# Performance work log

Measured on AMD Instinct MI355X. Metric: run time of the kernel, lower is better.

Reference implementation:

```python
import jax, jax.numpy as jnp
import numpy as np
from jax import lax

B, T, D, H, W = 2, 8, 64, 64, 64
E, HID = 4, 256


def _layernorm(x, g, b, eps=1e-5):
    m = x.mean(-1, keepdims=True)
    v = ((x - m) ** 2).mean(-1, keepdims=True)
    return (x - m) / jnp.sqrt(v + eps) * g + b


def _pscan(A, X, axis):
    # linear recurrence h_t = A_t * h_{t-1} + X_t via associative scan
    def comb(l, r):
        a1, x1 = l
        a2, x2 = r
        return a2 * a1, a2 * x1 + x2
    return lax.associative_scan(comb, (A, X), axis=axis)[1]


def setup_inputs() -> dict:
    key = jax.random.key(0)
    ks = jax.random.split(key, 32)
    r = lambda i, shape, s=1.0: jax.random.normal(ks[i], shape, jnp.float32) * s
    D2 = 2 * D
    return {
        'x_re': r(0, (B, T, D, H, W)), 'x_im': r(1, (B, T, D, H, W)),
        'dt': jax.random.uniform(ks[2], (T,), jnp.float32, 0.5, 1.0),
        'ln_s_g': jnp.ones(D2), 'ln_s_b': jnp.zeros(D2),
        'conv_w': r(3, (3, 3, D2, D2), 0.03), 'conv_b': jnp.zeros(D2),
        'mom_w': r(4, (D2, D2), 0.08), 'mom_b': jnp.zeros(D2),
        'adv_w': jnp.full((1,), 0.1, jnp.float32),
        'enc_re': r(5, (D, D), 0.1), 'enc_im': r(6, (D, D), 0.1),
        'dec_re': r(7, (D, D), 0.1), 'dec_im': r(8, (D, D), 0.1),
        'flux_a_re': r(9, (D,)), 'flux_a_im': r(10, (D,), 0.1),
        'fin_re': r(11, (D, D), 0.1), 'fin_im': r(12, (D, D), 0.1),
        'fproj_re': r(13, (D, D), 0.1), 'fproj_im': r(14, (D, D), 0.1),
        'gate_w': r(15, (D2, D), 0.1), 'gate_b': jnp.zeros(D),
        'lam_re': r(16, (D,)), 'lam_im': r(17, (D,), 0.1),
        'noise_re': r(18, (B, T, H, W, D)), 'noise_im': r(19, (B, T, H, W, D)),
        'e_scale': jnp.full((1,), 0.1, jnp.float32),
        'ln_t_g': jnp.ones(D2), 'ln_t_b': jnp.zeros(D2),
        'router_w': r(20, (D2, E), 0.1), 'router_b': jnp.zeros(E),
        'w1': r(21, (E, D2, HID), 0.08), 'b1': jnp.zeros((E, HID)),
        'w2': r(22, (E, HID, D2), 0.08), 'b2': jnp.zeros((E, D2)),
    }


def _forward(x_re, x_im, dt, ln_s_g, ln_s_b, conv_w, conv_b, mom_w, mom_b, adv_w,
             enc_re, enc_im, dec_re, dec_im, flux_a_re, flux_a_im, fin_re, fin_im,
             fproj_re, fproj_im, gate_w, gate_b, lam_re, lam_im, noise_re, noise_im,
             e_scale, ln_t_g, ln_t_b, router_w, router_b, w1, b1, w2, b2):
    x = (x_re + 1j * x_im).astype(jnp.complex64)            # [B,T,D,H,W]
    target_energy = (jnp.abs(x) ** 2).mean(axis=(-2, -1))   # [B,T,D]
    momentum = x.mean(axis=(-2, -1))                        # [B,T,D] complex
    xcl = jnp.transpose(x, (0, 1, 3, 4, 2))                 # [B,T,H,W,D]
    Bs, Ts, Hs, Ws, Ds = xcl.shape
    D2 = 2 * Ds
    # --- spatial complex (Clifford) conv branch: LN over 2D channels + conv ---
    xr = jnp.concatenate([xcl.real, xcl.imag], -1)          # [B,T,H,W,2D]
    xn = _layernorm(xr, ln_s_g, ln_s_b)
    y = lax.conv_general_dilated(xn.reshape(Bs * Ts, Hs, Ws, D2), conv_w,
                                 (1, 1), 'SAME',
                                 dimension_numbers=('NHWC', 'HWIO', 'NHWC')) + conv_b
    y = y.reshape(Bs, Ts, Hs, Ws, D2)
    xcl = xcl + (y[..., :Ds] + 1j * y[..., Ds:])
    # --- momentum advection ---
    z_mean = xcl.mean(axis=(2, 3))                          # [B,T,D]
    mom_cat = jnp.concatenate([momentum.real, momentum.imag], -1) @ mom_w + mom_b
    mom_new = mom_cat[..., :Ds] + 1j * mom_cat[..., Ds:]
    dtb = jnp.broadcast_to(dt[None, :], (Bs, Ts))
    xcl = xcl + (mom_new * adv_w[0])[:, :, None, None, :] * dtb[:, :, None, None, None]
    momentum = 0.9 * momentum + 0.1 * z_mean
    # --- eigenbasis encode ---
    x_eigen = xcl @ (enc_re + 1j * enc_im)                  # [B,T,H,W,D]
    x_mean = x_eigen.mean(axis=(2, 3))                      # [B,T,D]
    # --- flux tracker: parallel scan over T ---
    A_flux = jnp.exp(-jax.nn.softplus(flux_a_re) + 1j * flux_a_im)
    A_flux = jnp.broadcast_to(A_flux, (Bs, Ts, Ds)).astype(jnp.complex64)
    X_flux = x_mean @ (fin_re + 1j * fin_im)
    flux_seq = _pscan(A_flux, X_flux, axis=1)               # [B,T,D]
    source = flux_seq @ (fproj_re + 1j * fproj_im)
    gate = jax.nn.sigmoid(jnp.concatenate([flux_seq.real, flux_seq.imag], -1) @ gate_w + gate_b)
    g = gate[:, :, None, None, :]
    forcing = x_eigen * g + source[:, :, None, None, :] * (1.0 - g)
    # --- temporal propagation: per-site parallel scan over T ---
    lam = -jax.nn.softplus(lam_re) + 1j * lam_im            # [D]
    op_decay = jnp.exp(lam[None, None, :] * dtb[:, :, None])  # [B,T,D]
    op_forcing = (op_decay - 1.0) / lam
    u_t = forcing * op_forcing[:, :, None, None, :]
    A_time = jnp.broadcast_to(op_decay[:, :, None, None, :], u_t.shape)
    u_out = _pscan(A_time, u_t, axis=1)                     # [B,T,H,W,D]
    noise = 0.01 * jnp.sqrt(dtb)[:, :, None, None, None] * (noise_re + 1j * noise_im)
    u_out = u_out + noise
    # --- decode + energy projection ---
    x_out = u_out @ (dec_re + 1j * dec_im)                  # [B,T,H,W,D]
    cur_e = (jnp.abs(x_out) ** 2).mean(axis=(2, 3))
    ratio = jnp.clip(target_energy / (cur_e + 1e-8), 0.5, 2.0)
    sf = jnp.sqrt(ratio)[:, :, None, None, :]
    x_out = x_out * (1.0 + e_scale[0] * (sf - 1.0))
    # --- temporal LN + MoE FFN on real-concat tokens ---
    xr2 = jnp.concatenate([x_out.real, x_out.imag], -1)
    xn2 = _layernorm(xr2, ln_t_g, ln_t_b)                   # [B,T,H,W,2D]
    tok = xn2.reshape(-1, D2)                               # [N,2D]
    p = jax.nn.softmax(tok @ router_w + router_b, -1)       # [N,E]
    hmid = jax.nn.gelu(jnp.einsum('nd,edh->neh', tok, w1) + b1)
    eout = jnp.einsum('neh,ehd->ned', hmid, w2) + b2
    out_tok = tok + jnp.einsum('ne,ned->nd', p, eout)
    out = out_tok.reshape(Bs, Ts, Hs, Ws, D2)
    x_out_c = out[..., :Ds] + 1j * out[..., Ds:]
    z_out = xcl + x_out_c
    z = jnp.transpose(z_out, (0, 1, 4, 2, 3))               # [B,T,D,H,W]
    return jnp.stack([z.real, z.imag])                      # [2,B,T,D,H,W]


def reference(x_re, x_im, dt, ln_s_g, ln_s_b, conv_w, conv_b, mom_w, mom_b, adv_w,
              enc_re, enc_im, dec_re, dec_im, flux_a_re, flux_a_im, fin_re, fin_im,
              fproj_re, fproj_im, gate_w, gate_b, lam_re, lam_im, noise_re, noise_im,
              e_scale, ln_t_g, ln_t_b, router_w, router_b, w1, b1, w2, b2):
    return _forward(x_re, x_im, dt, ln_s_g, ln_s_b, conv_w, conv_b, mom_w, mom_b, adv_w,
                    enc_re, enc_im, dec_re, dec_im, flux_a_re, flux_a_im, fin_re, fin_im,
                    fproj_re, fproj_im, gate_w, gate_b, lam_re, lam_im, noise_re, noise_im,
                    e_scale, ln_t_g, ln_t_b, router_w, router_b, w1, b1, w2, b2)
```

## Files before the change

### kernel.cpp

```cpp
#include <hip/hip_runtime.h>
#include <hip/hip_bf16.h>
#include <math.h>


#define W_XB     4194304u
#define W_C      8388608u
#define W_CWT    12582912u
#define W_W1T    14680064u
#define W_W2T    14745600u
#define W_ENCM   14811136u
#define W_DECM   14819328u
#define W_XMP_RE 14827520u
#define W_XMP_IM 14893056u
#define W_EP_RE  14958592u
#define W_EP_IM  15220736u
#define W_EIG_RE 16777216u
#define W_K1R    20971520u
#define W_K1I    21037056u
#define W_K1E    21102592u
#define W_SMALL  25165824u
#define W_TE     (W_SMALL+0u)
#define W_MTRE   (W_SMALL+3072u)
#define W_MTIM   (W_SMALL+4096u)
#define W_GATE   (W_SMALL+5120u)
#define W_SRCRE  (W_SMALL+6144u)
#define W_SRCIM  (W_SMALL+7168u)
#define W_OPFRE  (W_SMALL+8192u)
#define W_OPFIM  (W_SMALL+9216u)
#define W_OPDRE  (W_SMALL+10240u)
#define W_OPDIM  (W_SMALL+11264u)
#define W_SCALE  (W_SMALL+12288u)

#define XB_IM 4194304u

typedef __attribute__((ext_vector_type(8))) short bf16x8;
typedef __attribute__((ext_vector_type(4))) float f32x4;

__device__ __forceinline__ unsigned short bfr(float x) {
  __hip_bfloat16 h = __float2bfloat16(x);
  return *(unsigned short*)&h;
}
__device__ __forceinline__ unsigned int pk2(float a, float b) {
  return ((unsigned int)bfr(b) << 16) | (unsigned int)bfr(a);
}
__device__ __forceinline__ float sb2f(short s) {
  return __uint_as_float(((unsigned int)(unsigned short)s) << 16);
}

__global__ __launch_bounds__(256) void k2_transpose_ln(
    const float* __restrict__ xre, const float* __restrict__ xim,
    const float* __restrict__ g, const float* __restrict__ bb_, float* ws) {
  int blk = blockIdx.x; int bt = blk >> 6, h = blk & 63;
  __shared__ float tre[64][65], tim[64][65];
  __shared__ float ps[4][64], pq[4][64], pe[4][64];
  __shared__ float mean_l[64], rstd_l[64];
  size_t inbase = (size_t)bt * 262144 + (size_t)h * 64;
  for (int i = threadIdx.x; i < 1024; i += 256) {
    int d = i >> 4, w4 = (i & 15) * 4;
    float4 vr = *(const float4*)&xre[inbase + (size_t)d * 4096 + w4];
    float4 vi = *(const float4*)&xim[inbase + (size_t)d * 4096 + w4];
    tre[d][w4] = vr.x; tre[d][w4 + 1] = vr.y; tre[d][w4 + 2] = vr.z; tre[d][w4 + 3] = vr.w;
    tim[d][w4] = vi.x; tim[d][w4 + 1] = vi.y; tim[d][w4 + 2] = vi.z; tim[d][w4 + 3] = vi.w;
  }
  __syncthreads();
  {
    int w = threadIdx.x & 63, part = threadIdx.x >> 6;
    float s = 0.f, sq = 0.f;
    for (int dd = part * 16; dd < part * 16 + 16; dd++) {
      float vr = tre[dd][w], vi = tim[dd][w];
      s += vr + vi; sq += vr * vr + vi * vi;
    }
    ps[part][w] = s; pq[part][w] = sq;
  }
  __syncthreads();
  if (threadIdx.x < 64) {
    int w = threadIdx.x;
    float s  = ps[0][w] + ps[1][w] + ps[2][w] + ps[3][w];
    float sq = pq[0][w] + pq[1][w] + pq[2][w] + pq[3][w];
    float m = s / 128.f;
    float v = sq / 128.f - m * m;
    mean_l[w] = m; rstd_l[w] = rsqrtf(v + 1e-5f);
  }
  __syncthreads();
  {
    int d = threadIdx.x & 63, part = threadIdx.x >> 6;
    float sr = 0.f, si = 0.f, se = 0.f;
    for (int w = part * 16; w < part * 16 + 16; w++) {
      float vr = tre[d][w], vi = tim[d][w];
      sr += vr; si += vi; se += vr * vr + vi * vi;
    }
    ps[part][d] = sr; pq[part][d] = si; pe[part][d] = se;
  }
  __syncthreads();
  if (threadIdx.x < 64) {
    int d = threadIdx.x;
    int idx = h * 1024 + bt * 64 + d;
    ws[W_K1R + idx] = ps[0][d] + ps[1][d] + ps[2][d] + ps[3][d];
    ws[W_K1I + idx] = pq[0][d] + pq[1][d] + pq[2][d] + pq[3][d];
    ws[W_K1E + idx] = pe[0][d] + pe[1][d] + pe[2][d] + pe[3][d];
  }
  {
    __hip_bfloat16* xbb = (__hip_bfloat16*)(ws + W_XB);
    for (int i = threadIdx.x; i < 1024; i += 256) {
      int d = i >> 4, w4 = (i & 15) * 4;
      size_t ob = (size_t)(bt * 64 + d) * 4096 + (size_t)h * 64 + w4;
      *(unsigned int*)&xbb[ob]     = pk2(tre[d][w4],     tre[d][w4 + 1]);
      *(unsigned int*)&xbb[ob + 2] = pk2(tre[d][w4 + 2], tre[d][w4 + 3]);
      *(unsigned int*)&xbb[XB_IM + ob]     = pk2(tim[d][w4],     tim[d][w4 + 1]);
      *(unsigned int*)&xbb[XB_IM + ob + 2] = pk2(tim[d][w4 + 2], tim[d][w4 + 3]);
    }
  }
  size_t tokbase = (size_t)blk * 64;
  __hip_bfloat16* xnb = (__hip_bfloat16*)(ws + W_C);
  int c0 = (threadIdx.x & 63) * 2, wg = threadIdx.x >> 6;
  float gc0 = g[c0], bc0 = bb_[c0], gc1 = g[c0 + 1], bc1 = bb_[c0 + 1];
  for (int pass = 0; pass < 16; pass++) {
    int w = pass * 4 + wg;
    float m = mean_l[w], rs = rstd_l[w];
    float v0 = (c0 < 64) ? tre[c0][w] : tim[c0 - 64][w];
    float v1 = (c0 + 1 < 64) ? tre[c0 + 1][w] : tim[c0 + 1 - 64][w];
    *(unsigned int*)&xnb[tokbase * 128 + (size_t)w * 128 + c0] =
        pk2((v0 - m) * rs * gc0 + bc0, (v1 - m) * rs * gc1 + bc1);
  }
}

__global__ void k1b2b(const float* __restrict__ mom_w, const float* __restrict__ mom_b,
                      const float* __restrict__ adv_w, const float* __restrict__ dt, float* ws) {
  int bt = blockIdx.x; int t = bt & 7;
  __shared__ float mc[128], outl[128];
  int tid = threadIdx.x;
  if (tid < 64) {
    int d = tid;
    float a = 0.f, b = 0.f, c = 0.f;
    for (int h = 0; h < 64; h++) {
      int idx = h * 1024 + bt * 64 + d;
      a += ws[W_K1R + idx]; b += ws[W_K1I + idx]; c += ws[W_K1E + idx];
    }
    ws[W_TE + bt * 64 + d] = c / 4096.f;
    mc[d] = a / 4096.f;
    mc[64 + d] = b / 4096.f;
  }
  __syncthreads();
  float acc = mom_b[tid];
  for (int k = 0; k < 128; k++) acc += mc[k] * mom_w[k * 128 + tid];
  outl[tid] = acc;
  __syncthreads();
  if (tid < 64) {
    float f = adv_w[0] * dt[t];
    ws[W_MTRE + bt * 64 + tid] = outl[tid] * f;
    ws[W_MTIM + bt * 64 + tid] = outl[64 + tid] * f;
  }
}

__global__ void k0_wprep(const float* __restrict__ w1, const float* __restrict__ w2,
                         const float* __restrict__ cw,
                         const float* __restrict__ enc_re, const float* __restrict__ enc_im,
                         const float* __restrict__ dec_re, const float* __restrict__ dec_im,
                         float* ws) {
  __hip_bfloat16* w1f = (__hip_bfloat16*)(ws + W_W1T);
  __hip_bfloat16* w2f = (__hip_bfloat16*)(ws + W_W2T);
  __hip_bfloat16* cwt = (__hip_bfloat16*)(ws + W_CWT);
  __hip_bfloat16* encM = (__hip_bfloat16*)(ws + W_ENCM);
  __hip_bfloat16* decM = (__hip_bfloat16*)(ws + W_DECM);
  int idx = blockIdx.x * 256 + threadIdx.x;
  if (idx < 131072) {
    {
      int j = idx & 7, lane = (idx >> 3) & 63, kt = (idx >> 9) & 3, nt = (idx >> 11) & 15, e = idx >> 15;
      int cout = nt * 16 + (lane & 15);
      int cin = kt * 32 + (lane >> 4) * 8 + j;
      w1f[idx] = __float2bfloat16(w1[((size_t)(e * 128 + cin)) * 256 + cout]);
    }
    {
      int j = idx & 7, lane = (idx >> 3) & 63, kt = (idx >> 9) & 7, nt = (idx >> 12) & 7, e = idx >> 15;
      int cout = nt * 16 + (lane & 15);
      int cin = kt * 32 + (lane >> 4) * 8 + j;
      w2f[idx] = __float2bfloat16(w2[((size_t)(e * 256 + cin)) * 128 + cout]);
    }
  }
  if (idx < 147456) {
    int j = idx & 7, lane = (idx >> 3) & 63, kt = (idx >> 9) & 3, r = idx >> 11;
    int nt = r & 7, tap = r >> 3;
    int cout = nt * 16 + (lane & 15);
    int cin = kt * 32 + (lane >> 4) * 8 + j;
    cwt[idx] = __float2bfloat16(cw[((size_t)(tap * 128 + cin)) * 128 + cout]);
  }
  if (idx < 16384) {
    int jj = idx & 7, lane = (idx >> 3) & 63, kt = (idx >> 9) & 3, nt = idx >> 11;
    int jc = nt * 16 + (lane & 15);
    int k = kt * 32 + (lane >> 4) * 8 + jj;
    float ve, vd;
    if (k < 64) {
      ve = (jc < 64) ? enc_re[k * 64 + jc] : enc_im[k * 64 + (jc - 64)];
      vd = (jc < 64) ? dec_re[k * 64 + jc] : dec_im[k * 64 + (jc - 64)];
    } else {
      int kk = k - 64;
      ve = (jc < 64) ? -enc_im[kk * 64 + jc] : enc_re[kk * 64 + (jc - 64)];
      vd = (jc < 64) ? -dec_im[kk * 64 + jc] : dec_re[kk * 64 + (jc - 64)];
    }
    encM[idx] = __float2bfloat16(ve);
    decM[idx] = __float2bfloat16(vd);
  }
}

__global__ __launch_bounds__(256) void k3_conv_enc(const float* __restrict__ cb, float* ws) {
  int blk = blockIdx.x; int bt = blk >> 6, h = blk & 63;
  const __hip_bfloat16* xnb = (const __hip_bfloat16*)(ws + W_C);
  const __hip_bfloat16* cwt = (const __hip_bfloat16*)(ws + W_CWT);
  const __hip_bfloat16* encM = (const __hip_bfloat16*)(ws + W_ENCM);
  const __hip_bfloat16* xbb = (const __hip_bfloat16*)(ws + W_XB);
  __hip_bfloat16* xclb = (__hip_bfloat16*)ws;
  __hip_bfloat16* eigb = (__hip_bfloat16*)(ws + W_EIG_RE);
  __shared__ __align__(16) char smem[3 * 66 * 136 * 2];
  __hip_bfloat16 (*xin)[66][136] = (__hip_bfloat16(*)[66][136])smem;
  char* A = smem;
  int tid = threadIdx.x, lane = tid & 63, wv = tid >> 6;
  int arow = lane & 15, kgrp = (lane >> 4) * 8, rbase = (lane >> 4) * 4;

  for (int r = 0; r < 3; r++) {
    int hh = h + r - 1;
    if (hh < 0 || hh >= 64) {
      unsigned int* z = (unsigned int*)&xin[r][0][0];
      for (int i = tid; i < 4488; i += 256) z[i] = 0u;
    } else {
      if (tid < 68) *(unsigned int*)&xin[r][0][tid * 2] = 0u;
      else if (tid < 136) *(unsigned int*)&xin[r][65][(tid - 136 + 68) * 2] = 0u;
      const __hip_bfloat16* src = xnb + ((size_t)bt * 4096 + (size_t)hh * 64) * 128;
      for (int i = tid; i < 1024; i += 256) {
        int wp = (i >> 4) + 1, c8 = (i & 15) * 8;
        *(bf16x8*)&xin[r][wp][c8] = *(const bf16x8*)&src[(size_t)(wp - 1) * 128 + c8];
      }
    }
  }
  __syncthreads();

  f32x4 oacc[4][2];
  #pragma unroll
  for (int m = 0; m < 4; m++) {
    oacc[m][0] = (f32x4){0.f, 0.f, 0.f, 0.f};
    oacc[m][1] = (f32x4){0.f, 0.f, 0.f, 0.f};
  }

  for (int tap = 0; tap < 9; tap++) {
    int kh = tap / 3, kw = tap % 3;
    const __hip_bfloat16* wt0 = cwt + ((size_t)(tap * 8 + wv * 2) * 4) * 512 + lane * 8;
    #pragma unroll
    for (int kt = 0; kt < 4; kt++) {
      bf16x8 a[4];
      #pragma unroll
      for (int m = 0; m < 4; m++)
        a[m] = *(const bf16x8*)&xin[kh][m * 16 + arow + kw][kt * 32 + kgrp];
      bf16x8 b0 = *(const bf16x8*)&wt0[(size_t)kt * 512];
      bf16x8 b1 = *(const bf16x8*)&wt0[(size_t)(kt + 4) * 512];
      #pragma unroll
      for (int m = 0; m < 4; m++) {
        oacc[m][0] = __builtin_amdgcn_mfma_f32_16x16x32_bf16(a[m], b0, oacc[m][0], 0, 0, 0);
        oacc[m][1] = __builtin_amdgcn_mfma_f32_16x16x32_bf16(a[m], b1, oacc[m][1], 0, 0, 0);
      }
    }
  }
  __syncthreads();

  size_t rowtok = (size_t)blk * 64;
  #pragma unroll
  for (int n = 0; n < 2; n++) {
    int cout = (wv * 2 + n) * 16 + arow;
    bool isre = cout < 64;
    int d = cout & 63;
    float add = cb[cout] + ws[(isre ? W_MTRE : W_MTIM) + bt * 64 + d];
    size_t xb = isre ? 0u : XB_IM;
    const __hip_bfloat16* xsrc = xbb + xb + (size_t)(bt * 64 + d) * 4096 + (size_t)h * 64;
    #pragma unroll
    for (int m = 0; m < 4; m++) {
      unsigned int u0 = *(const unsigned int*)&xsrc[m * 16 + rbase];
      unsigned int u1 = *(const unsigned int*)&xsrc[m * 16 + rbase + 2];
      float xo0 = __uint_as_float(u0 << 16);
      float xo1 = __uint_as_float(u0 & 0xffff0000u);
      float xo2 = __uint_as_float(u1 << 16);
      float xo3 = __uint_as_float(u1 & 0xffff0000u);
      #pragma unroll
      for (int r = 0; r < 4; r++) {
        int w = m * 16 + rbase + r;
        float xo = (r == 0) ? xo0 : (r == 1) ? xo1 : (r == 2) ? xo2 : xo3;
        float v = xo + oacc[m][n][r] + add;
        xclb[xb + (rowtok + w) * 64 + d] = __float2bfloat16(v);
        *(__hip_bfloat16*)(A + w * 256 + ((cout * 2) ^ ((w & 7) << 4))) = __float2bfloat16(v);
      }
    }
  }
  __syncthreads();

  f32x4 acc[4][2];
  #pragma unroll
  for (int m = 0; m < 4; m++) {
    acc[m][0] = (f32x4){0.f, 0.f, 0.f, 0.f};
    acc[m][1] = (f32x4){0.f, 0.f, 0.f, 0.f};
  }
  #pragma unroll
  for (int kt = 0; kt < 4; kt++) {
    bf16x8 a[4];
    #pragma unroll
    for (int m = 0; m < 4; m++)
      a[m] = *(const bf16x8*)(A + (m * 16 + arow) * 256 + (((kt * 32 + kgrp) * 2) ^ ((arow & 7) << 4)));
    bf16x8 b0 = *(const bf16x8*)&encM[(((size_t)(wv * 2 + 0) * 4 + kt) * 64 + lane) * 8];
    bf16x8 b1 = *(const bf16x8*)&encM[(((size_t)(wv * 2 + 1) * 4 + kt) * 64 + lane) * 8];
    #pragma unroll
    for (int m = 0; m < 4; m++) {
      acc[m][0] = __builtin_amdgcn_mfma_f32_16x16x32_bf16(a[m], b0, acc[m][0], 0, 0, 0);
      acc[m][1] = __builtin_amdgcn_mfma_f32_16x16x32_bf16(a[m], b1, acc[m][1], 0, 0, 0);
    }
  }
  #pragma unroll
  for (int n = 0; n < 2; n++) {
    int jc = (wv * 2 + n) * 16 + arow;
    size_t eb = (jc < 64) ? 0u : XB_IM;
    int col = jc & 63;
    #pragma unroll
    for (int m = 0; m < 4; m++)
      #pragma unroll
      for (int r = 0; r < 4; r++)
        eigb[eb + (rowtok + m * 16 + rbase + r) * 64 + col] = __float2bfloat16(acc[m][n][r]);
    float s = 0.f;
    #pragma unroll
    for (int m = 0; m < 4; m++)
      #pragma unroll
      for (int r = 0; r < 4; r++) s += acc[m][n][r];
    s += __shfl_xor(s, 16);
    s += __shfl_xor(s, 32);
    if (lane < 16)
      ws[(jc < 64 ? W_XMP_RE : W_XMP_IM) + (size_t)blk * 64 + col] = s;
  }
}

__device__ __forceinline__ float softplusf(float x) {
  return (x > 20.f) ? x : log1pf(expf(x));
}

__global__ void k6_seq(const float* __restrict__ fin_re, const float* __restrict__ fin_im,
                       const float* __restrict__ fproj_re, const float* __restrict__ fproj_im,
                       const float* __restrict__ flux_a_re, const float* __restrict__ flux_a_im,
                       const float* __restrict__ gate_w, const float* __restrict__ gate_b,
                       const float* __restrict__ lam_re, const float* __restrict__ lam_im,
                       const float* __restrict__ dt, float* ws) {
  __shared__ float xmr[1024], xmi[1024], Xfr[1024], Xfi[1024], flr[1024], fli[1024];
  int tid = threadIdx.x;
  for (int i = tid; i < 1024; i += 256) {
    int bt = i >> 6, j = i & 63;
    float sr = 0.f, si = 0.f;
    for (int q = 0; q < 64; q++) {
      sr += ws[W_XMP_RE + (size_t)(bt * 64 + q) * 64 + j];
      si += ws[W_XMP_IM + (size_t)(bt * 64 + q) * 64 + j];
    }
    xmr[i] = sr / 4096.f; xmi[i] = si / 4096.f;
  }
  __syncthreads();
  for (int i = tid; i < 1024; i += 256) {
    int bt = i >> 6, j = i & 63;
    float ar = 0.f, ai = 0.f;
    for (int d = 0; d < 64; d++) {
      float xr = xmr[bt * 64 + d], xi = xmi[bt * 64 + d];
      float wr = fin_re[d * 64 + j], wi = fin_im[d * 64 + j];
      ar += xr * wr - xi * wi; ai += xr * wi + xi * wr;
    }
    Xfr[i] = ar; Xfi[i] = ai;
  }
  __syncthreads();
  if (tid < 128) {
    int b = tid >> 6, j = tid & 63;
    float mag = expf(-softplusf(flux_a_re[j]));
    float aar = mag * cosf(flux_a_im[j]), aai = mag * sinf(flux_a_im[j]);
    float sr = 0.f, si = 0.f;
    for (int t = 0; t < 8; t++) {
      int idx = (b * 8 + t) * 64 + j;
      float nr = aar * sr - aai * si + Xfr[idx];
      float ni = aar * si + aai * sr + Xfi[idx];
      sr = nr; si = ni;
      flr[idx] = sr; fli[idx] = si;
    }
  }
  __syncthreads();
  for (int i = tid; i < 1024; i += 256) {
    int bt = i >> 6, j = i & 63;
    float ar = 0.f, ai = 0.f, lg = 0.f;
    for (int d = 0; d < 64; d++) {
      float fr = flr[bt * 64 + d], fi = fli[bt * 64 + d];
      float wr = fproj_re[d * 64 + j], wi = fproj_im[d * 64 + j];
      ar += fr * wr - fi * wi; ai += fr * wi + fi * wr;
      lg += fr * gate_w[d * 64 + j] + fi * gate_w[(64 + d) * 64 + j];
    }
    ws[W_SRCRE + i] = ar; ws[W_SRCIM + i] = ai;
    ws[W_GATE + i] = 1.f / (1.f + expf(-(lg + gate_b[j])));
  }
  for (int i = tid; i < 1024; i += 256) {
    int bt = i >> 6, d = i & 63, t = bt & 7;
    float lr = -softplusf(lam_re[d]), li = lam_im[d];
    float dtv = dt[t];
    float mag = expf(lr * dtv);
    float dr = mag * cosf(li * dtv), di = mag * sinf(li * dtv);
    ws[W_OPDRE + i] = dr; ws[W_OPDIM + i] = di;
    float omr = dr - 1.f, omi = di;
    float den = lr * lr + li * li;
    ws[W_OPFRE + i] = (omr * lr + omi * li) / den;
    ws[W_OPFIM + i] = (omi * lr - omr * li) / den;
  }
}

__global__ __launch_bounds__(256) void k7_dec(const float* __restrict__ nre,
                                              const float* __restrict__ nim,
                                              const float* __restrict__ dt, float* ws) {
  int blk = blockIdx.x;
  int b = blk >> 8, h = (blk >> 2) & 63, wq = blk & 3;
  const __hip_bfloat16* decM = (const __hip_bfloat16*)(ws + W_DECM);
  __hip_bfloat16* eigb = (__hip_bfloat16*)(ws + W_EIG_RE);
  __shared__ float gl[8][64], srl[8][64], sil[8][64], ofr[8][64], ofi[8][64], odr[8][64], odi[8][64];
  __shared__ __align__(16) char A[2][4096];
  __shared__ float dts[8];
  int tid = threadIdx.x, lane = tid & 63, wv = tid >> 6;
  int arow = lane & 15, kgrp = (lane >> 4) * 8, rbase = (lane >> 4) * 4;
  for (int i = tid; i < 512; i += 256) {
    int t = i >> 6, d = i & 63, idx = (b * 8 + t) * 64 + d;
    gl[t][d]  = ws[W_GATE + idx];
    srl[t][d] = ws[W_SRCRE + idx]; sil[t][d] = ws[W_SRCIM + idx];
    ofr[t][d] = ws[W_OPFRE + idx]; ofi[t][d] = ws[W_OPFIM + idx];
    odr[t][d] = ws[W_OPDRE + idx]; odi[t][d] = ws[W_OPDIM + idx];
  }
  if (tid < 8) dts[tid] = dt[tid];
  __syncthreads();

  int dp = (tid & 31) * 2, wslot = tid >> 5;
  float ur[2][2], ui[2][2];
  #pragma unroll
  for (int a_ = 0; a_ < 2; a_++) { ur[a_][0] = 0.f; ur[a_][1] = 0.f; ui[a_][0] = 0.f; ui[a_][1] = 0.f; }

  for (int t = 0; t < 8; t++) {
    float ns = 0.01f * sqrtf(dts[t]);
    size_t tokb = ((size_t)(b * 8 + t) * 64 + h) * 64 + (size_t)wq * 16;
    char* At = A[t & 1];
    float g0 = gl[t][dp],  g1 = gl[t][dp + 1];
    float s0 = srl[t][dp], s1 = srl[t][dp + 1];
    float q0 = sil[t][dp], q1 = sil[t][dp + 1];
    float f0 = ofr[t][dp], f1 = ofr[t][dp + 1];
    float e0 = ofi[t][dp], e1 = ofi[t][dp + 1];
    float r0 = odr[t][dp], r1 = odr[t][dp + 1];
    float o0 = odi[t][dp], o1 = odi[t][dp + 1];
    #pragma unroll
    for (int wi = 0; wi < 2; wi++) {
      int wl = wslot + wi * 8;
      size_t off = (tokb + wl) * 64 + dp;
      unsigned int re2 = *(const unsigned int*)&eigb[off];
      unsigned int im2 = *(const unsigned int*)&eigb[XB_IM + off];
      float2 nr2 = *(const float2*)&nre[off];
      float2 ni2 = *(const float2*)&nim[off];
      float uo0, vo0, uo1, vo1;
      {
        float er_ = __uint_as_float(re2 << 16);
        float ei_ = __uint_as_float(im2 << 16);
        float fre = er_ * g0 + s0 * (1.f - g0);
        float fim = ei_ * g0 + q0 * (1.f - g0);
        float utr = fre * f0 - fim * e0;
        float uti = fre * e0 + fim * f0;
        float nur = r0 * ur[wi][0] - o0 * ui[wi][0] + utr;
        float nui = r0 * ui[wi][0] + o0 * ur[wi][0] + uti;
        ur[wi][0] = nur; ui[wi][0] = nui;
        uo0 = nur + ns * nr2.x; vo0 = nui + ns * ni2.x;
      }
      {
        float er_ = __uint_as_float(re2 & 0xffff0000u);
        float ei_ = __uint_as_float(im2 & 0xffff0000u);
        float fre = er_ * g1 + s1 * (1.f - g1);
        float fim = ei_ * g1 + q1 * (1.f - g1);
        float utr = fre * f1 - fim * e1;
        float uti = fre * e1 + fim * f1;
        float nur = r1 * ur[wi][1] - o1 * ui[wi][1] + utr;
        float nui = r1 * ui[wi][1] + o1 * ur[wi][1] + uti;
        ur[wi][1] = nur; ui[wi][1] = nui;
        uo1 = nur + ns * nr2.y; vo1 = nui + ns * ni2.y;
      }
      int sw = (wl & 7) << 4;
      *(unsigned int*)(At + wl * 256 + ((dp * 2) ^ sw)) = pk2(uo0, uo1);
      *(unsigned int*)(At + wl * 256 + ((128 + dp * 2) ^ sw)) = pk2(vo0, vo1);
    }
    __syncthreads();
    f32x4 acc[2];
    acc[0] = (f32x4){0.f, 0.f, 0.f, 0.f};
    acc[1] = (f32x4){0.f, 0.f, 0.f, 0.f};
    #pragma unroll
    for (int kt = 0; kt < 4; kt++) {
      bf16x8 a0 = *(const bf16x8*)(At + arow * 256 + (((kt * 32 + kgrp) * 2) ^ ((arow & 7) << 4)));
      bf16x8 b0 = *(const bf16x8*)&decM[(((size_t)(wv * 2 + 0) * 4 + kt) * 64 + lane) * 8];
      bf16x8 b1 = *(const bf16x8*)&decM[(((size_t)(wv * 2 + 1) * 4 + kt) * 64 + lane) * 8];
      acc[0] = __builtin_amdgcn_mfma_f32_16x16x32_bf16(a0, b0, acc[0], 0, 0, 0);
      acc[1] = __builtin_amdgcn_mfma_f32_16x16x32_bf16(a0, b1, acc[1], 0, 0, 0);
    }
    #pragma unroll
    for (int n = 0; n < 2; n++) {
      int jc = (wv * 2 + n) * 16 + arow;
      size_t eb = (jc < 64) ? 0u : XB_IM;
      int col = jc & 63;
      #pragma unroll
      for (int r = 0; r < 4; r++)
        eigb[eb + (tokb + rbase + r) * 64 + col] = __float2bfloat16(acc[n][r]);
      float s = acc[n][0] * acc[n][0] + acc[n][1] * acc[n][1]
              + acc[n][2] * acc[n][2] + acc[n][3] * acc[n][3];
      s += __shfl_xor(s, 16);
      s += __shfl_xor(s, 32);
      if (lane < 16)
        ws[(jc < 64 ? W_EP_RE : W_EP_IM)
           + (size_t)((b * 8 + t) * 256 + h * 4 + wq) * 64 + col] = s;
    }
  }
}

__global__ void k9b_scale(const float* __restrict__ escale, float* ws) {
  int bt = blockIdx.x; int j = threadIdx.x;
  float s = 0.f;
  for (int q = 0; q < 256; q++) {
    size_t idx = (size_t)(bt * 256 + q) * 64 + j;
    s += ws[W_EP_RE + idx] + ws[W_EP_IM + idx];
  }
  float cur = s / 4096.f;
  float te = ws[W_TE + bt * 64 + j];
  float ratio = te / (cur + 1e-8f);
  ratio = fminf(fmaxf(ratio, 0.5f), 2.0f);
  ws[W_SCALE + bt * 64 + j] = 1.f + escale[0] * (sqrtf(ratio) - 1.f);
}

__global__ __launch_bounds__(512) void k11_moe(
    const float* __restrict__ rw, const float* __restrict__ rb,
    const float* __restrict__ b1, const float* __restrict__ b2,
    const float* __restrict__ g2, const float* __restrict__ b2_,
    float* __restrict__ ws, float* __restrict__ out) {
  int blk = blockIdx.x; int bt = blk >> 6, h = blk & 63;
  const __hip_bfloat16* w1f = (const __hip_bfloat16*)(ws + W_W1T);
  const __hip_bfloat16* w2f = (const __hip_bfloat16*)(ws + W_W2T);
  const __hip_bfloat16* xclb = (const __hip_bfloat16*)ws;
  const __hip_bfloat16* eigb = (const __hip_bfloat16*)(ws + W_EIG_RE);
  __shared__ __align__(16) char smem[147456];
  __shared__ float pl[64][4];
  char* lt = smem;
  int tid = threadIdx.x, lane = tid & 63, wv = tid >> 6;
  int arow = lane & 15, kgrp = (lane >> 4) * 8, rbase = (lane >> 4) * 4;
  size_t tokbase = (size_t)blk * 64;

  int w = tid >> 3, part = tid & 7;
  int c0 = part * 16, dbase = (part & 3) * 16;
  const __hip_bfloat16* rp = eigb + ((part < 4) ? 0u : XB_IM) + (tokbase + w) * 64 + dbase;
  const float* scg = ws + W_SCALE + bt * 64 + dbase;
  float an[16];
  {
    bf16x8 h0 = *(const bf16x8*)rp;
    bf16x8 h1 = *(const bf16x8*)(rp + 8);
    float f[16];
    #pragma unroll
    for (int j = 0; j < 8; j++) {
      f[j]     = sb2f(h0[j]) * scg[j];
      f[8 + j] = sb2f(h1[j]) * scg[8 + j];
    }
    float s = 0.f, sq = 0.f;
    #pragma unroll
    for (int k = 0; k < 16; k++) { s += f[k]; sq += f[k] * f[k]; }
    s  += __shfl_xor(s, 1);  s  += __shfl_xor(s, 2);  s  += __shfl_xor(s, 4);
    sq += __shfl_xor(sq, 1); sq += __shfl_xor(sq, 2); sq += __shfl_xor(sq, 4);
    float m = s / 128.f, v = sq / 128.f - m * m;
    float rstd = rsqrtf(v + 1e-5f);
    int szw = (w & 7) << 4;
    #pragma unroll
    for (int q = 0; q < 4; q++) {
      int c = c0 + q * 4;
      float a0 = (f[q * 4 + 0] - m) * rstd * g2[c]     + b2_[c];
      float a1 = (f[q * 4 + 1] - m) * rstd * g2[c + 1] + b2_[c + 1];
      float a2 = (f[q * 4 + 2] - m) * rstd * g2[c + 2] + b2_[c + 2];
      float a3 = (f[q * 4 + 3] - m) * rstd * g2[c + 3] + b2_[c + 3];
      an[q * 4 + 0] = a0; an[q * 4 + 1] = a1; an[q * 4 + 2] = a2; an[q * 4 + 3] = a3;
      *(unsigned int*)(lt + w * 256 + ((c * 2) ^ szw)) = pk2(a0, a1);
      *(unsigned int*)(lt + w * 256 + (((c + 2) * 2) ^ szw)) = pk2(a2, a3);
    }
    float l0 = 0.f, l1 = 0.f, l2 = 0.f, l3 = 0.f;
    #pragma unroll
    for (int k = 0; k < 16; k++) {
      float4 r4 = *(const float4*)&rw[(c0 + k) * 4];
      l0 += an[k] * r4.x; l1 += an[k] * r4.y; l2 += an[k] * r4.z; l3 += an[k] * r4.w;
    }
    l0 += __shfl_xor(l0, 1); l0 += __shfl_xor(l0, 2); l0 += __shfl_xor(l0, 4);
    l1 += __shfl_xor(l1, 1); l1 += __shfl_xor(l1, 2); l1 += __shfl_xor(l1, 4);
    l2 += __shfl_xor(l2, 1); l2 += __shfl_xor(l2, 2); l2 += __shfl_xor(l2, 4);
    l3 += __shfl_xor(l3, 1); l3 += __shfl_xor(l3, 2); l3 += __shfl_xor(l3, 4);
    l0 += rb[0]; l1 += rb[1]; l2 += rb[2]; l3 += rb[3];
    float mx = fmaxf(fmaxf(l0, l1), fmaxf(l2, l3));
    float e0 = expf(l0 - mx), e1 = expf(l1 - mx), e2 = expf(l2 - mx), e3 = expf(l3 - mx);
    float rs = __builtin_amdgcn_rcpf(e0 + e1 + e2 + e3);
    if (part == 0) {
      float4 p; p.x = e0 * rs; p.y = e1 * rs; p.z = e2 * rs; p.w = e3 * rs;
      *(float4*)&pl[w][0] = p;
    }
  }
  __syncthreads();

  f32x4 oacc[4];
  #pragma unroll
  for (int m = 0; m < 4; m++) {
    int col = wv * 16 + arow;
    oacc[m] = (f32x4){0.f, 0.f, 0.f, 0.f};
    #pragma unroll
    for (int r = 0; r < 4; r++) {
      int row = m * 16 + rbase + r;
      oacc[m][r] = __bfloat162float(
          *(const __hip_bfloat16*)(lt + row * 256 + ((col * 2) ^ ((row & 7) << 4))));
    }
  }

  for (int e = 0; e < 4; e++) {
    char* hb = smem + 16384 + e * 32768;
    f32x4 acc1[4][2];
    #pragma unroll
    for (int m = 0; m < 4; m++) {
      acc1[m][0] = (f32x4){0.f, 0.f, 0.f, 0.f};
      acc1[m][1] = (f32x4){0.f, 0.f, 0.f, 0.f};
    }
    #pragma unroll
    for (int kt = 0; kt < 4; kt++) {
      bf16x8 a[4];
      #pragma unroll
      for (int m = 0; m < 4; m++) {
        int row = m * 16 + arow;
        a[m] = *(const bf16x8*)(lt + row * 256 + (((kt * 32 + kgrp) * 2) ^ ((arow & 7) << 4)));
      }
      bf16x8 b0 = *(const bf16x8*)&w1f[(((size_t)(e * 16 + wv * 2 + 0) * 4 + kt) * 64 + lane) * 8];
      bf16x8 b1 = *(const bf16x8*)&w1f[(((size_t)(e * 16 + wv * 2 + 1) * 4 + kt) * 64 + lane) * 8];
      #pragma unroll
      for (int m = 0; m < 4; m++) {
        acc1[m][0] = __builtin_amdgcn_mfma_f32_16x16x32_bf16(a[m], b0, acc1[m][0], 0, 0, 0);
        acc1[m][1] = __builtin_amdgcn_mfma_f32_16x16x32_bf16(a[m], b1, acc1[m][1], 0, 0, 0);
      }
    }
    #pragma unroll
    for (int n = 0; n < 2; n++) {
      int col = (wv * 2 + n) * 16 + arow;
      float bv = b1[e * 256 + col];
      #pragma unroll
      for (int m = 0; m < 4; m++)
        #pragma unroll
        for (int r = 0; r < 4; r++) {
          float hv = acc1[m][n][r] + bv;
          float z = 1.5957691216f * hv + 0.0713548162f * hv * hv * hv;
          float gelu = hv * __builtin_amdgcn_rcpf(1.f + __expf(-z));
          int row = m * 16 + rbase + r;
          *(__hip_bfloat16*)(hb + row * 512 + ((col * 2) ^ ((row & 7) << 4))) =
              __float2bfloat16(gelu);
        }
    }
  }
  __syncthreads();

  for (int e = 0; e < 4; e++) {
    const char* hb = smem + 16384 + e * 32768;
    f32x4 acc2[4];
    #pragma unroll
    for (int m = 0; m < 4; m++) acc2[m] = (f32x4){0.f, 0.f, 0.f, 0.f};
    #pragma unroll
    for (int kt = 0; kt < 8; kt++) {
      bf16x8 a2[4];
      #pragma unroll
      for (int m = 0; m < 4; m++) {
        int row = m * 16 + arow;
        a2[m] = *(const bf16x8*)(hb + row * 512 + (((kt * 32 + kgrp) * 2) ^ ((arow & 7) << 4)));
      }
      bf16x8 bb = *(const bf16x8*)&w2f[(((size_t)(e * 8 + wv) * 8 + kt) * 64 + lane) * 8];
      #pragma unroll
      for (int m = 0; m < 4; m++)
        acc2[m] = __builtin_amdgcn_mfma_f32_16x16x32_bf16(a2[m], bb, acc2[m], 0, 0, 0);
    }
    {
      int col = wv * 16 + arow;
      float bv2 = b2[e * 128 + col];
      #pragma unroll
      for (int m = 0; m < 4; m++)
        #pragma unroll
        for (int r = 0; r < 4; r++)
          oacc[m][r] += pl[m * 16 + rbase + r][e] * (acc2[m][r] + bv2);
    }
  }

  {
    int col = wv * 16 + arow;
    size_t xb = (col < 64) ? 0u : XB_IM;
    int dd = col & 63;
    size_t obase = (size_t)(col >> 6) * 4194304 + (size_t)bt * 262144
                 + (size_t)dd * 4096 + (size_t)h * 64;
    #pragma unroll
    for (int m = 0; m < 4; m++) {
      int wtb = m * 16 + rbase;
      float4 v;
      #pragma unroll
      for (int r = 0; r < 4; r++) {
        float res = __bfloat162float(xclb[xb + (tokbase + wtb + r) * 64 + dd]);
        ((float*)&v)[r] = oacc[m][r] + res;
      }
      *(float4*)&out[obase + wtb] = v;
    }
  }
}

extern "C" void kernel_launch(void* const* d_in, const int* in_sizes, int n_in,
                              void* d_out, int out_size, void* d_ws, size_t ws_size,
                              hipStream_t stream) {
  const float* x_re      = (const float*)d_in[0];
  const float* x_im      = (const float*)d_in[1];
  const float* dt        = (const float*)d_in[2];
  const float* ln_s_g    = (const float*)d_in[3];
  const float* ln_s_b    = (const float*)d_in[4];
  const float* conv_w    = (const float*)d_in[5];
  const float* conv_b    = (const float*)d_in[6];
  const float* mom_w     = (const float*)d_in[7];
  const float* mom_b     = (const float*)d_in[8];
  const float* adv_w     = (const float*)d_in[9];
  const float* enc_re    = (const float*)d_in[10];
  const float* enc_im    = (const float*)d_in[11];
  const float* dec_re    = (const float*)d_in[12];
  const float* dec_im    = (const float*)d_in[13];
  const float* flux_a_re = (const float*)d_in[14];
  const float* flux_a_im = (const float*)d_in[15];
  const float* fin_re    = (const float*)d_in[16];
  const float* fin_im    = (const float*)d_in[17];
  const float* fproj_re  = (const float*)d_in[18];
  const float* fproj_im  = (const float*)d_in[19];
  const float* gate_w    = (const float*)d_in[20];
  const float* gate_b    = (const float*)d_in[21];
  const float* lam_re    = (const float*)d_in[22];
  const float* lam_im    = (const float*)d_in[23];
  const float* noise_re  = (const float*)d_in[24];
  const float* noise_im  = (const float*)d_in[25];
  const float* e_scale   = (const float*)d_in[26];
  const float* ln_t_g    = (const float*)d_in[27];
  const float* ln_t_b    = (const float*)d_in[28];
  const float* router_w  = (const float*)d_in[29];
  const float* router_b  = (const float*)d_in[30];
  const float* w1        = (const float*)d_in[31];
  const float* b1        = (const float*)d_in[32];
  const float* w2        = (const float*)d_in[33];
  const float* b2        = (const float*)d_in[34];
  float* ws  = (float*)d_ws;
  float* out = (float*)d_out;

  k0_wprep<<<576, 256, 0, stream>>>(w1, w2, conv_w, enc_re, enc_im, dec_re, dec_im, ws);
  k2_transpose_ln<<<1024, 256, 0, stream>>>(x_re, x_im, ln_s_g, ln_s_b, ws);
  k1b2b<<<16, 128, 0, stream>>>(mom_w, mom_b, adv_w, dt, ws);
  k3_conv_enc<<<1024, 256, 0, stream>>>(conv_b, ws);
  k6_seq<<<1, 256, 0, stream>>>(fin_re, fin_im, fproj_re, fproj_im, flux_a_re, flux_a_im,
                                gate_w, gate_b, lam_re, lam_im, dt, ws);
  k7_dec<<<512, 256, 0, stream>>>(noise_re, noise_im, dt, ws);
  k9b_scale<<<16, 64, 0, stream>>>(e_scale, ws);
  k11_moe<<<1024, 512, 0, stream>>>(router_w, router_b, b1, b2, ln_t_g, ln_t_b, ws, out);
}
```

Before: 239.1 us.

## Split single-block sequential kernel into parallel stages and use shuffle reductions in LN

The single-block k6_seq kernel is split into three kernels: a 16-block mean reduction, a single-block flux recurrence, and a 16-block gate/projection kernel that uses a 4-way split with shuffle reductions. This spreads the serial small-matrix work across more compute units. Intermediate results now pass through global workspace, and the two extra launches add launch overhead. Separately, k2_transpose_ln replaces its shared-memory partial sums and two barriers with wave shuffle reductions.

```diff
diff --git a/kernel.cpp b/kernel.cpp
--- a/kernel.cpp
+++ b/kernel.cpp
@@ -14,6 +14,10 @@
 #define W_XMP_IM 14893056u
 #define W_EP_RE  14958592u
 #define W_EP_IM  15220736u
+#define W_XMR    15482880u
+#define W_XMI    15483904u
+#define W_FLR    15484928u
+#define W_FLI    15485952u
 #define W_EIG_RE 16777216u
 #define W_K1R    20971520u
 #define W_K1I    21037056u
@@ -46,16 +50,19 @@
 __device__ __forceinline__ float sb2f(short s) {
   return __uint_as_float(((unsigned int)(unsigned short)s) << 16);
 }
+__device__ __forceinline__ float softplusf(float x) {
+  return (x > 20.f) ? x : log1pf(expf(x));
+}
 
 __global__ __launch_bounds__(256) void k2_transpose_ln(
     const float* __restrict__ xre, const float* __restrict__ xim,
     const float* __restrict__ g, const float* __restrict__ bb_, float* ws) {
   int blk = blockIdx.x; int bt = blk >> 6, h = blk & 63;
   __shared__ float tre[64][65], tim[64][65];
-  __shared__ float ps[4][64], pq[4][64], pe[4][64];
   __shared__ float mean_l[64], rstd_l[64];
+  int tid = threadIdx.x;
   size_t inbase = (size_t)bt * 262144 + (size_t)h * 64;
-  for (int i = threadIdx.x; i < 1024; i += 256) {
+  for (int i = tid; i < 1024; i += 256) {
     int d = i >> 4, w4 = (i & 15) * 4;
     float4 vr = *(const float4*)&xre[inbase + (size_t)d * 4096 + w4];
     float4 vi = *(const float4*)&xim[inbase + (size_t)d * 4096 + w4];
@@ -64,44 +71,37 @@
   }
   __syncthreads();
   {
-    int w = threadIdx.x & 63, part = threadIdx.x >> 6;
+    int w = tid >> 2, part = tid & 3;
     float s = 0.f, sq = 0.f;
     for (int dd = part * 16; dd < part * 16 + 16; dd++) {
       float vr = tre[dd][w], vi = tim[dd][w];
       s += vr + vi; sq += vr * vr + vi * vi;
     }
-    ps[part][w] = s; pq[part][w] = sq;
-  }
-  __syncthreads();
-  if (threadIdx.x < 64) {
-    int w = threadIdx.x;
-    float s  = ps[0][w] + ps[1][w] + ps[2][w] + ps[3][w];
-    float sq = pq[0][w] + pq[1][w] + pq[2][w] + pq[3][w];
-    float m = s / 128.f;
-    float v = sq / 128.f - m * m;
-    mean_l[w] = m; rstd_l[w] = rsqrtf(v + 1e-5f);
-  }
-  __syncthreads();
+    s += __shfl_xor(s, 1);  s += __shfl_xor(s, 2);
+    sq += __shfl_xor(sq, 1); sq += __shfl_xor(sq, 2);
+    if (part == 0) {
+      float m = s / 128.f, v = sq / 128.f - m * m;
+      mean_l[w] = m; rstd_l[w] = rsqrtf(v + 1e-5f);
+    }
+  }
   {
-    int d = threadIdx.x & 63, part = threadIdx.x >> 6;
+    int d = tid >> 2, part = tid & 3;
     float sr = 0.f, si = 0.f, se = 0.f;
-    for (int w = part * 16; w < part * 16 + 16; w++) {
-      float vr = tre[d][w], vi = tim[d][w];
+    for (int w2 = part * 16; w2 < part * 16 + 16; w2++) {
+      float vr = tre[d][w2], vi = tim[d][w2];
       sr += vr; si += vi; se += vr * vr + vi * vi;
     }
-    ps[part][d] = sr; pq[part][d] = si; pe[part][d] = se;
-  }
-  __syncthreads();
-  if (threadIdx.x < 64) {
-    int d = threadIdx.x;
-    int idx = h * 1024 + bt * 64 + d;
-    ws[W_K1R + idx] = ps[0][d] + ps[1][d] + ps[2][d] + ps[3][d];
-    ws[W_K1I + idx] = pq[0][d] + pq[1][d] + pq[2][d] + pq[3][d];
-    ws[W_K1E + idx] = pe[0][d] + pe[1][d] + pe[2][d] + pe[3][d];
+    sr += __shfl_xor(sr, 1); sr += __shfl_xor(sr, 2);
+    si += __shfl_xor(si, 1); si += __shfl_xor(si, 2);
+    se += __shfl_xor(se, 1); se += __shfl_xor(se, 2);
+    if (part == 0) {
+      int idx = h * 1024 + bt * 64 + d;
+      ws[W_K1R + idx] = sr; ws[W_K1I + idx] = si; ws[W_K1E + idx] = se;
+    }
   }
   {
     __hip_bfloat16* xbb = (__hip_bfloat16*)(ws + W_XB);
-    for (int i = threadIdx.x; i < 1024; i += 256) {
+    for (int i = tid; i < 1024; i += 256) {
       int d = i >> 4, w4 = (i & 15) * 4;
       size_t ob = (size_t)(bt * 64 + d) * 4096 + (size_t)h * 64 + w4;
       *(unsigned int*)&xbb[ob]     = pk2(tre[d][w4],     tre[d][w4 + 1]);
@@ -110,9 +110,10 @@
       *(unsigned int*)&xbb[XB_IM + ob + 2] = pk2(tim[d][w4 + 2], tim[d][w4 + 3]);
     }
   }
+  __syncthreads();
   size_t tokbase = (size_t)blk * 64;
   __hip_bfloat16* xnb = (__hip_bfloat16*)(ws + W_C);
-  int c0 = (threadIdx.x & 63) * 2, wg = threadIdx.x >> 6;
+  int c0 = (tid & 63) * 2, wg = tid >> 6;
   float gc0 = g[c0], bc0 = bb_[c0], gc1 = g[c0 + 1], bc1 = bb_[c0 + 1];
   for (int pass = 0; pass < 16; pass++) {
     int w = pass * 4 + wg;
@@ -331,33 +332,27 @@
   }
 }
 
-__device__ __forceinline__ float softplusf(float x) {
-  return (x > 20.f) ? x : log1pf(expf(x));
-}
-
-__global__ void k6_seq(const float* __restrict__ fin_re, const float* __restrict__ fin_im,
-                       const float* __restrict__ fproj_re, const float* __restrict__ fproj_im,
-                       const float* __restrict__ flux_a_re, const float* __restrict__ flux_a_im,
-                       const float* __restrict__ gate_w, const float* __restrict__ gate_b,
-                       const float* __restrict__ lam_re, const float* __restrict__ lam_im,
-                       const float* __restrict__ dt, float* ws) {
-  __shared__ float xmr[1024], xmi[1024], Xfr[1024], Xfi[1024], flr[1024], fli[1024];
+__global__ void k6a_xm(float* ws) {
+  int bt = blockIdx.x, j = threadIdx.x;
+  float sr = 0.f, si = 0.f;
+  for (int q = 0; q < 64; q++) {
+    sr += ws[W_XMP_RE + (size_t)(bt * 64 + q) * 64 + j];
+    si += ws[W_XMP_IM + (size_t)(bt * 64 + q) * 64 + j];
+  }
+  ws[W_XMR + bt * 64 + j] = sr / 4096.f;
+  ws[W_XMI + bt * 64 + j] = si / 4096.f;
+}
+
+__global__ void k6b_flux(const float* __restrict__ fin_re, const float* __restrict__ fin_im,
+                         const float* __restrict__ flux_a_re, const float* __restrict__ flux_a_im,
+                         float* ws) {
+  __shared__ float Xfr[1024], Xfi[1024];
   int tid = threadIdx.x;
-  for (int i = tid; i < 1024; i += 256) {
-    int bt = i >> 6, j = i & 63;
-    float sr = 0.f, si = 0.f;
-    for (int q = 0; q < 64; q++) {
-      sr += ws[W_XMP_RE + (size_t)(bt * 64 + q) * 64 + j];
-      si += ws[W_XMP_IM + (size_t)(bt * 64 + q) * 64 + j];
-    }
-    xmr[i] = sr / 4096.f; xmi[i] = si / 4096.f;
-  }
-  __syncthreads();
   for (int i = tid; i < 1024; i += 256) {
     int bt = i >> 6, j = i & 63;
     float ar = 0.f, ai = 0.f;
     for (int d = 0; d < 64; d++) {
-      float xr = xmr[bt * 64 + d], xi = xmi[bt * 64 + d];
+      float xr = ws[W_XMR + bt * 64 + d], xi = ws[W_XMI + bt * 64 + d];
       float wr = fin_re[d * 64 + j], wi = fin_im[d * 64 + j];
       ar += xr * wr - xi * wi; ai += xr * wi + xi * wr;
     }
@@ -374,33 +369,48 @@
       float nr = aar * sr - aai * si + Xfr[idx];
       float ni = aar * si + aai * sr + Xfi[idx];
       sr = nr; si = ni;
-      flr[idx] = sr; fli[idx] = si;
-    }
-  }
-  __syncthreads();
-  for (int i = tid; i < 1024; i += 256) {
-    int bt = i >> 6, j = i & 63;
-    float ar = 0.f, ai = 0.f, lg = 0.f;
-    for (int d = 0; d < 64; d++) {
-      float fr = flr[bt * 64 + d], fi = fli[bt * 64 + d];
-      float wr = fproj_re[d * 64 + j], wi = fproj_im[d * 64 + j];
-      ar += fr * wr - fi * wi; ai += fr * wi + fi * wr;
-      lg += fr * gate_w[d * 64 + j] + fi * gate_w[(64 + d) * 64 + j];
-    }
-    ws[W_SRCRE + i] = ar; ws[W_SRCIM + i] = ai;
-    ws[W_GATE + i] = 1.f / (1.f + expf(-(lg + gate_b[j])));
-  }
-  for (int i = tid; i < 1024; i += 256) {
-    int bt = i >> 6, d = i & 63, t = bt & 7;
+      ws[W_FLR + idx] = sr; ws[W_FLI + idx] = si;
+    }
+  }
+}
+
+__global__ void k6c_gate(const float* __restrict__ fproj_re, const float* __restrict__ fproj_im,
+                         const float* __restrict__ gate_w, const float* __restrict__ gate_b,
+                         const float* __restrict__ lam_re, const float* __restrict__ lam_im,
+                         const float* __restrict__ dt, float* ws) {
+  int bt = blockIdx.x;
+  __shared__ float flr[64], fli[64];
+  int tid = threadIdx.x;
+  if (tid < 64) { flr[tid] = ws[W_FLR + bt * 64 + tid]; fli[tid] = ws[W_FLI + bt * 64 + tid]; }
+  __syncthreads();
+  int j = tid >> 2, part = tid & 3;
+  float ar = 0.f, ai = 0.f, lg = 0.f;
+  for (int d = part * 16; d < part * 16 + 16; d++) {
+    float fr = flr[d], fi = fli[d];
+    float wr = fproj_re[d * 64 + j], wi = fproj_im[d * 64 + j];
+    ar += fr * wr - fi * wi; ai += fr * wi + fi * wr;
+    lg += fr * gate_w[d * 64 + j] + fi * gate_w[(64 + d) * 64 + j];
+  }
+  ar += __shfl_xor(ar, 1); ar += __shfl_xor(ar, 2);
+  ai += __shfl_xor(ai, 1); ai += __shfl_xor(ai, 2);
+  lg += __shfl_xor(lg, 1); lg += __shfl_xor(lg, 2);
+  if (part == 0) {
+    int idx = bt * 64 + j;
+    ws[W_SRCRE + idx] = ar; ws[W_SRCIM + idx] = ai;
+    ws[W_GATE + idx] = 1.f / (1.f + expf(-(lg + gate_b[j])));
+  }
+  if (tid < 64) {
+    int d = tid, t = bt & 7;
     float lr = -softplusf(lam_re[d]), li = lam_im[d];
     float dtv = dt[t];
     float mag = expf(lr * dtv);
     float dr = mag * cosf(li * dtv), di = mag * sinf(li * dtv);
-    ws[W_OPDRE + i] = dr; ws[W_OPDIM + i] = di;
+    int idx = bt * 64 + d;
+    ws[W_OPDRE + idx] = dr; ws[W_OPDIM + idx] = di;
     float omr = dr - 1.f, omi = di;
     float den = lr * lr + li * li;
-    ws[W_OPFRE + i] = (omr * lr + omi * li) / den;
-    ws[W_OPFIM + i] = (omi * lr - omr * li) / den;
+    ws[W_OPFRE + idx] = (omr * lr + omi * li) / den;
+    ws[W_OPFIM + idx] = (omi * lr - omr * li) / den;
   }
 }
 
@@ -745,8 +755,9 @@
   k2_transpose_ln<<<1024, 256, 0, stream>>>(x_re, x_im, ln_s_g, ln_s_b, ws);
   k1b2b<<<16, 128, 0, stream>>>(mom_w, mom_b, adv_w, dt, ws);
   k3_conv_enc<<<1024, 256, 0, stream>>>(conv_b, ws);
-  k6_seq<<<1, 256, 0, stream>>>(fin_re, fin_im, fproj_re, fproj_im, flux_a_re, flux_a_im,
-                                gate_w, gate_b, lam_re, lam_im, dt, ws);
+  k6a_xm<<<16, 64, 0, stream>>>(ws);
+  k6b_flux<<<1, 256, 0, stream>>>(fin_re, fin_im, flux_a_re, flux_a_im, ws);
+  k6c_gate<<<16, 256, 0, stream>>>(fproj_re, fproj_im, gate_w, gate_b, lam_re, lam_im, dt, ws);
   k7_dec<<<512, 256, 0, stream>>>(noise_re, noise_im, dt, ws);
   k9b_scale<<<16, 64, 0, stream>>>(e_scale, ws);
   k11_moe<<<1024, 512, 0, stream>>>(router_w, router_b, b1, b2, ln_t_g, ln_t_b, ws, out);
```

Measured after the change: 227.0 us. 5.1% less time.
